# Kernel tuning notes

Hardware: AMD Instinct MI355X
Metric: run time of the kernel (lower is better)

The kernel has to match this reference:

```python
import jax, jax.numpy as jnp
import numpy as np

B, C, H, W = 4, 512, 64, 64
KEY_DIM, VALUE_DIM = 512, 512


def setup_inputs() -> dict:
    key = jax.random.key(0)
    k1, k2, k3, k4 = jax.random.split(key, 4)
    s = 1.0 / np.sqrt(C).astype(np.float32)
    x = jax.random.normal(k1, (B, C, H, W), jnp.float32)
    # torch nn.Linear weights have shape (out_features, in_features)
    Wk = jax.random.normal(k2, (KEY_DIM, C), jnp.float32) * s
    Wq = jax.random.normal(k3, (KEY_DIM, C), jnp.float32) * s
    Wv = jax.random.normal(k4, (VALUE_DIM, C), jnp.float32) * s
    return {"x": x, "Wk": Wk, "Wq": Wq, "Wv": Wv}


def reference(x, Wk, Wq, Wv):
    b, c, h, w = x.shape
    kd = Wk.shape[0]
    n = h * w
    # (b,c,h,w) -> (b, n, c) tokens, matching transpose+flatten in the original
    xt = x.transpose(0, 2, 3, 1).reshape(b, n, c)
    q = xt @ Wq.T  # (b, n, kd)
    k = xt @ Wk.T  # (b, n, kd)
    v = xt @ Wv.T  # (b, n, vd)
    scaling = np.sqrt(float(kd)).astype(np.float32)
    scores = jax.nn.softmax(jnp.einsum('bnd,bmd->bnm', q, k) / scaling, axis=-1)
    # original: output[j] = sum_i values[i] * scores[j, i]  ==  scores @ V
    out = jnp.einsum('bnm,bmv->bnv', scores, v)  # (b, n, vd)
    # original scores_out: sum over dim=0 (query index) of the (n, n) score matrix
    scores_out = scores.sum(axis=1).reshape(b, 1, h, w)
    out = out.reshape(b, h, w, -1).transpose(0, 3, 1, 2)  # (b, vd, h, w)
    return out, scores_out
```

## Files before the change

### kernel.cpp

```cpp
#include <hip/hip_runtime.h>


typedef short bf16x8 __attribute__((ext_vector_type(8)));
typedef float f32x4 __attribute__((ext_vector_type(4)));

#define NTOK 4096
#define DDIM 512
#define NB   4

__device__ __forceinline__ unsigned short f32_bf16(float f) {
  union { float f; unsigned u; } v; v.f = f;
  unsigned r = v.u + 0x7FFFu + ((v.u >> 16) & 1u);
  return (unsigned short)(r >> 16);
}

__device__ __forceinline__ float bf16_f32(short s) {
  union { unsigned u; float f; } v;
  v.u = ((unsigned)(unsigned short)s) << 16;
  return v.f;
}

__global__ __launch_bounds__(256, 4) void qkv_proj(
    const float* __restrict__ x,
    const float* __restrict__ Wq,
    const float* __restrict__ Wk,
    const float* __restrict__ Wv,
    unsigned short* __restrict__ Qt,
    unsigned short* __restrict__ Kf,
    unsigned short* __restrict__ Vt)
{
  const int nt0 = blockIdx.x * 64;
  const int d0  = blockIdx.y * 64;
  const int b   = blockIdx.z;
  const int tid = threadIdx.x;
  const int wave = tid >> 6;
  const int lane = tid & 63;
  const int l15  = lane & 15;
  const int quad = lane >> 4;

  __shared__ __align__(16) unsigned short Xt[64 * 40];
  __shared__ __align__(16) unsigned short Wl[3][64 * 40];

  f32x4 aq[4], ak[4], av[4];
#pragma unroll
  for (int i = 0; i < 4; ++i) {
    aq[i] = (f32x4){0.f,0.f,0.f,0.f};
    ak[i] = (f32x4){0.f,0.f,0.f,0.f};
    av[i] = (f32x4){0.f,0.f,0.f,0.f};
  }

  const float* xb = x + (size_t)b * DDIM * NTOK + nt0;
  const int xn  = tid & 63;
  const int xc8 = tid >> 6;
  const int wc8 = tid & 3;
  const int wdd = tid >> 2;

  for (int cc = 0; cc < DDIM; cc += 32) {
    __syncthreads();
    {
      bf16x8 t;
#pragma unroll
      for (int j = 0; j < 8; ++j)
        t[j] = (short)f32_bf16(xb[(size_t)(cc + xc8 * 8 + j) * NTOK + xn]);
      *(bf16x8*)(&Xt[xn * 40 + xc8 * 8]) = t;
    }
    {
      const float* wsrc[3] = {Wq, Wk, Wv};
#pragma unroll
      for (int m = 0; m < 3; ++m) {
        const float* src = wsrc[m] + (size_t)(d0 + wdd) * DDIM + cc + wc8 * 8;
        bf16x8 t;
#pragma unroll
        for (int j = 0; j < 8; ++j) t[j] = (short)f32_bf16(src[j]);
        *(bf16x8*)(&Wl[m][wdd * 40 + wc8 * 8]) = t;
      }
    }
    __syncthreads();

    bf16x8 xa  = *(const bf16x8*)(&Xt[(wave * 16 + l15) * 40 + quad * 8]);
    bf16x8 wva = *(const bf16x8*)(&Wl[2][(wave * 16 + l15) * 40 + quad * 8]);
#pragma unroll
    for (int nt = 0; nt < 4; ++nt) {
      bf16x8 wqf = *(const bf16x8*)(&Wl[0][(nt * 16 + l15) * 40 + quad * 8]);
      bf16x8 wkf = *(const bf16x8*)(&Wl[1][(nt * 16 + l15) * 40 + quad * 8]);
      bf16x8 xbf = *(const bf16x8*)(&Xt[(nt * 16 + l15) * 40 + quad * 8]);
      aq[nt] = __builtin_amdgcn_mfma_f32_16x16x32_bf16(xa,  wqf, aq[nt], 0, 0, 0);
      ak[nt] = __builtin_amdgcn_mfma_f32_16x16x32_bf16(xa,  wkf, ak[nt], 0, 0, 0);
      av[nt] = __builtin_amdgcn_mfma_f32_16x16x32_bf16(wva, xbf, av[nt], 0, 0, 0);
    }
  }

#pragma unroll
  for (int nt = 0; nt < 4; ++nt) {
#pragma unroll
    for (int r = 0; r < 4; ++r) {
      const int tokq = nt0 + wave * 16 + quad * 4 + r;
      const int dq   = d0 + nt * 16 + l15;
      Qt[((size_t)b * NTOK + tokq) * DDIM + dq] = f32_bf16(aq[nt][r]);
      {
        const int kblk  = (nt0 >> 4) + wave;
        const int dc    = (d0 >> 5) + (nt >> 1);
        const int laneK = ((nt & 1) * 2 + (l15 >> 3)) * 16 + quad * 4 + r;
        Kf[((size_t)(b * 256 + kblk) * 16 + dc) * 512 + laneK * 8 + (l15 & 7)] =
            f32_bf16(ak[nt][r]);
      }
      const int dblk  = (d0 >> 4) + wave;
      const int ic    = (nt0 >> 5) + (nt >> 1);
      const int laneV = ((nt & 1) * 2 + (l15 >> 3)) * 16 + quad * 4 + r;
      Vt[(size_t)b * DDIM * NTOK +
         ((size_t)(dblk * 128 + ic) * 64 + laneV) * 8 + (l15 & 7)] =
          f32_bf16(av[nt][r]);
    }
  }
}

#define SCALE 0.044194173824159216f

__global__ __launch_bounds__(256, 2) void attn_lsum_p(
    const unsigned short* __restrict__ Qt,
    const unsigned short* __restrict__ Kf,
    unsigned short* __restrict__ Pt,
    float* __restrict__ lsum_g)
{
  const int qb = blockIdx.x;
  const int kp = blockIdx.y;
  const int b  = blockIdx.z;
  const int tid  = threadIdx.x;
  const int wave = tid >> 6;
  const int lane = tid & 63;
  const int l15  = lane & 15;
  const int quad = lane >> 4;
  const int q0   = qb * 128 + wave * 32;

  __shared__ __align__(16) unsigned short Klds[64 * 512];

  bf16x8 qf[2][16];
#pragma unroll
  for (int qt = 0; qt < 2; ++qt) {
    const unsigned short* qp =
        Qt + ((size_t)b * NTOK + q0 + qt * 16 + l15) * DDIM + quad * 8;
#pragma unroll
    for (int dc = 0; dc < 16; ++dc) qf[qt][dc] = *(const bf16x8*)(qp + dc * 32);
  }

  unsigned short* Pq = Pt + (size_t)b * NTOK * NTOK +
                       (size_t)(qb * 2 + (wave >> 1)) * 262144;
  const int ntb = (wave & 1) * 2;

  float ls[2][4] = {{0.f,0.f,0.f,0.f},{0.f,0.f,0.f,0.f}};

  for (int kc = 0; kc < 16; ++kc) {
    const int kblk0 = kp * 64 + kc * 4;
    __syncthreads();
    {
      const unsigned short* src = Kf + ((size_t)(b * 256 + kblk0) * 16) * 512;
#pragma unroll
      for (int it = 0; it < 16; ++it) {
        const int idx = (tid + it * 256) * 8;
        *(bf16x8*)(&Klds[idx]) = *(const bf16x8*)(src + idx);
      }
    }
    __syncthreads();

#pragma unroll
    for (int kt = 0; kt < 4; ++kt) {
      const int kabs = kblk0 + kt;
      f32x4 s0 = (f32x4){0.f,0.f,0.f,0.f};
      f32x4 s1 = (f32x4){0.f,0.f,0.f,0.f};
#pragma unroll
      for (int dc = 0; dc < 16; ++dc) {
        const bf16x8 kbf = *(const bf16x8*)(&Klds[(kt * 16 + dc) * 512 + lane * 8]);
        s0 = __builtin_amdgcn_mfma_f32_16x16x32_bf16(qf[0][dc], kbf, s0, 0, 0, 0);
        s1 = __builtin_amdgcn_mfma_f32_16x16x32_bf16(qf[1][dc], kbf, s1, 0, 0, 0);
      }
      const int ic    = kabs >> 1;
      const int lt_hi = ((kabs & 1) * 2 + (l15 >> 3)) * 16;
      const int jj    = l15 & 7;
#pragma unroll
      for (int r = 0; r < 4; ++r) {
        const float e0 = __expf(s0[r] * SCALE);
        const float e1 = __expf(s1[r] * SCALE);
        ls[0][r] += e0;
        ls[1][r] += e1;
        Pq[((size_t)(ic * 4 + ntb) * 64 + lt_hi + quad * 4 + r) * 8 + jj] =
            f32_bf16(e0);
        Pq[((size_t)(ic * 4 + ntb + 1) * 64 + lt_hi + quad * 4 + r) * 8 + jj] =
            f32_bf16(e1);
      }
    }
  }

#pragma unroll
  for (int qt = 0; qt < 2; ++qt)
#pragma unroll
    for (int r = 0; r < 4; ++r) {
      float v = ls[qt][r];
      v += __shfl_xor(v, 1);
      v += __shfl_xor(v, 2);
      v += __shfl_xor(v, 4);
      v += __shfl_xor(v, 8);
      if (l15 == 0)
        unsafeAtomicAdd(&lsum_g[(size_t)b * NTOK + q0 + qt * 16 + quad * 4 + r], v);
    }
}

__global__ __launch_bounds__(256, 4) void attn_pv(
    const unsigned short* __restrict__ Pt,
    const unsigned short* __restrict__ Vt,
    const float* __restrict__ lsum_g,
    float* __restrict__ out,
    float* __restrict__ scores_out)
{
  const int q0b   = blockIdx.x;
  const int dpart = blockIdx.y;
  const int b     = blockIdx.z;
  const int tid  = threadIdx.x;
  const int wave = tid >> 6;
  const int lane = tid & 63;
  const int l15  = lane & 15;
  const int quad = lane >> 4;

  const int dblk0 = dpart * 8 + wave * 2;
  const unsigned short* Pq =
      Pt + (size_t)b * NTOK * NTOK + (size_t)q0b * 262144 + lane * 8;
  const unsigned short* Vp0 =
      Vt + (size_t)b * DDIM * NTOK + (size_t)(dblk0 + 0) * 65536 + lane * 8;
  const unsigned short* Vp1 =
      Vt + (size_t)b * DDIM * NTOK + (size_t)(dblk0 + 1) * 65536 + lane * 8;
  float* scb = scores_out + (size_t)b * NTOK;

  float rlv[4];
#pragma unroll
  for (int nt = 0; nt < 4; ++nt)
    rlv[nt] = 1.0f / lsum_g[(size_t)b * NTOK + q0b * 64 + nt * 16 + l15];

  f32x4 o[2][4];
#pragma unroll
  for (int i = 0; i < 2; ++i)
#pragma unroll
    for (int j = 0; j < 4; ++j) o[i][j] = (f32x4){0.f,0.f,0.f,0.f};

  bf16x8 pA[4], pB[4], vA[2], vB[2];

#define LOADP(D_, IC_)                                                         \
  do {                                                                         \
    _Pragma("unroll") for (int nt = 0; nt < 4; ++nt)                           \
      D_[nt] = *(const bf16x8*)(Pq + (size_t)(IC_)*2048 + nt * 512);           \
  } while (0)

#define LOADV(D_, IC_)                                                         \
  do {                                                                         \
    D_[0] = *(const bf16x8*)(Vp0 + (size_t)(IC_)*512);                         \
    D_[1] = *(const bf16x8*)(Vp1 + (size_t)(IC_)*512);                         \
  } while (0)

#define PV_COMPUTE(P_, V_, IC_)                                                \
  do {                                                                         \
    _Pragma("unroll") for (int mt = 0; mt < 2; ++mt)                           \
      _Pragma("unroll") for (int nt = 0; nt < 4; ++nt)                         \
        o[mt][nt] = __builtin_amdgcn_mfma_f32_16x16x32_bf16(                   \
            V_[mt], P_[nt], o[mt][nt], 0, 0, 0);                               \
    if ((((IC_) >> 5) == dpart) && ((((IC_) >> 3) & 3) == wave)) {             \
      float cj[8];                                                             \
      _Pragma("unroll") for (int j = 0; j < 8; ++j) cj[j] = 0.f;               \
      _Pragma("unroll") for (int nt = 0; nt < 4; ++nt)                         \
        _Pragma("unroll") for (int j = 0; j < 8; ++j)                          \
          cj[j] = fmaf(bf16_f32(P_[nt][j]), rlv[nt], cj[j]);                   \
      _Pragma("unroll") for (int j = 0; j < 8; ++j) {                          \
        float v_ = cj[j];                                                      \
        v_ += __shfl_xor(v_, 1);                                               \
        v_ += __shfl_xor(v_, 2);                                               \
        v_ += __shfl_xor(v_, 4);                                               \
        v_ += __shfl_xor(v_, 8);                                               \
        cj[j] = v_;                                                            \
      }                                                                        \
      if (l15 == 0) {                                                          \
        _Pragma("unroll") for (int j = 0; j < 8; ++j)                          \
          unsafeAtomicAdd(&scb[(IC_)*32 + quad * 8 + j], cj[j]);               \
      }                                                                        \
    }                                                                          \
  } while (0)

  LOADP(pA, 0); LOADV(vA, 0);
  LOADP(pB, 1); LOADV(vB, 1);

  for (int ic = 0; ic < 124; ic += 2) {
    PV_COMPUTE(pA, vA, ic);
    LOADP(pA, ic + 2); LOADV(vA, ic + 2);
    PV_COMPUTE(pB, vB, ic + 1);
    LOADP(pB, ic + 3); LOADV(vB, ic + 3);
  }
  PV_COMPUTE(pA, vA, 124);
  LOADP(pA, 126); LOADV(vA, 126);
  PV_COMPUTE(pB, vB, 125);
  LOADP(pB, 127); LOADV(vB, 127);
  PV_COMPUTE(pA, vA, 126);
  PV_COMPUTE(pB, vB, 127);

#undef LOADP
#undef LOADV
#undef PV_COMPUTE

  float* ob = out + ((size_t)b * DDIM + dpart * 128 + wave * 32) * NTOK + q0b * 64;
#pragma unroll
  for (int mt = 0; mt < 2; ++mt)
#pragma unroll
    for (int nt = 0; nt < 4; ++nt)
#pragma unroll
      for (int r = 0; r < 4; ++r)
        ob[(size_t)(mt * 16 + quad * 4 + r) * NTOK + nt * 16 + l15] =
            o[mt][nt][r] * rlv[nt];
}

extern "C" void kernel_launch(void* const* d_in, const int* in_sizes, int n_in,
                              void* d_out, int out_size, void* d_ws, size_t ws_size,
                              hipStream_t stream) {
  const float* x  = (const float*)d_in[0];
  const float* Wk = (const float*)d_in[1];
  const float* Wq = (const float*)d_in[2];
  const float* Wv = (const float*)d_in[3];

  float* out = (float*)d_out;
  float* scores_out = out + (size_t)NB * DDIM * NTOK;

  const size_t mat_elems = (size_t)NB * NTOK * DDIM;
  unsigned short* Qt = (unsigned short*)d_ws;
  unsigned short* Kf = Qt + mat_elems;
  unsigned short* Vt = Kf + mat_elems;
  float* lbuf = (float*)(Vt + mat_elems);
  unsigned short* Pt = (unsigned short*)(lbuf + (size_t)NB * NTOK);

  hipMemsetAsync(lbuf, 0, (size_t)NB * NTOK * sizeof(float), stream);
  hipMemsetAsync(scores_out, 0, (size_t)NB * NTOK * sizeof(float), stream);

  dim3 g1(NTOK / 64, DDIM / 64, NB);
  qkv_proj<<<g1, 256, 0, stream>>>(x, Wq, Wk, Wv, Qt, Kf, Vt);

  dim3 g2(NTOK / 128, 4, NB);
  attn_lsum_p<<<g2, 256, 0, stream>>>(Qt, Kf, Pt, lbuf);

  dim3 g3(NTOK / 64, 4, NB);
  attn_pv<<<g3, 256, 0, stream>>>(Pt, Vt, lbuf, out, scores_out);
}
```

Before: 404.8 us.

## Widen attn_pv tile to 64 value dims per wave with deeper prefetch

Each wave of the P@V kernel now computes 64 value dimensions instead of 32, and the grid's dpart dimension drops from 4 to 2. Each P tile loaded from global memory is therefore reused across twice as many MFMAs, halving total reads of the large P matrix. The software pipeline also deepens from 2 to 4 stages, and the scores_out ownership mapping is adjusted to match. The cost is many more registers (launch bounds lowered to 2 blocks per SM), so occupancy drops and fewer blocks are launched.

```diff
diff --git a/kernel.cpp b/kernel.cpp
--- a/kernel.cpp
+++ b/kernel.cpp
@@ -204,7 +204,7 @@
     }
 }
 
-__global__ __launch_bounds__(256, 4) void attn_pv(
+__global__ __launch_bounds__(256, 2) void attn_pv(
     const unsigned short* __restrict__ Pt,
     const unsigned short* __restrict__ Vt,
     const float* __restrict__ lsum_g,
@@ -220,27 +220,27 @@
   const int l15  = lane & 15;
   const int quad = lane >> 4;
 
-  const int dblk0 = dpart * 8 + wave * 2;
+  const int dblk0 = dpart * 16 + wave * 4;
   const unsigned short* Pq =
       Pt + (size_t)b * NTOK * NTOK + (size_t)q0b * 262144 + lane * 8;
-  const unsigned short* Vp0 =
-      Vt + (size_t)b * DDIM * NTOK + (size_t)(dblk0 + 0) * 65536 + lane * 8;
-  const unsigned short* Vp1 =
-      Vt + (size_t)b * DDIM * NTOK + (size_t)(dblk0 + 1) * 65536 + lane * 8;
+  const unsigned short* Vb =
+      Vt + (size_t)b * DDIM * NTOK + lane * 8;
   float* scb = scores_out + (size_t)b * NTOK;
+  const int sown = dpart * 4 + wave;
 
   float rlv[4];
 #pragma unroll
   for (int nt = 0; nt < 4; ++nt)
     rlv[nt] = 1.0f / lsum_g[(size_t)b * NTOK + q0b * 64 + nt * 16 + l15];
 
-  f32x4 o[2][4];
-#pragma unroll
-  for (int i = 0; i < 2; ++i)
+  f32x4 o[4][4];
+#pragma unroll
+  for (int i = 0; i < 4; ++i)
 #pragma unroll
     for (int j = 0; j < 4; ++j) o[i][j] = (f32x4){0.f,0.f,0.f,0.f};
 
-  bf16x8 pA[4], pB[4], vA[2], vB[2];
+  bf16x8 p0[4], p1[4], p2[4], p3[4];
+  bf16x8 v0[4], v1[4], v2[4], v3[4];
 
 #define LOADP(D_, IC_)                                                         \
   do {                                                                         \
@@ -250,17 +250,18 @@
 
 #define LOADV(D_, IC_)                                                         \
   do {                                                                         \
-    D_[0] = *(const bf16x8*)(Vp0 + (size_t)(IC_)*512);                         \
-    D_[1] = *(const bf16x8*)(Vp1 + (size_t)(IC_)*512);                         \
+    _Pragma("unroll") for (int mt = 0; mt < 4; ++mt)                           \
+      D_[mt] = *(const bf16x8*)(Vb + (size_t)(dblk0 + mt) * 65536 +            \
+                                (size_t)(IC_)*512);                            \
   } while (0)
 
-#define PV_COMPUTE(P_, V_, IC_)                                                \
+#define COMP(P_, V_, IC_)                                                      \
   do {                                                                         \
-    _Pragma("unroll") for (int mt = 0; mt < 2; ++mt)                           \
+    _Pragma("unroll") for (int mt = 0; mt < 4; ++mt)                           \
       _Pragma("unroll") for (int nt = 0; nt < 4; ++nt)                         \
         o[mt][nt] = __builtin_amdgcn_mfma_f32_16x16x32_bf16(                   \
             V_[mt], P_[nt], o[mt][nt], 0, 0, 0);                               \
-    if ((((IC_) >> 5) == dpart) && ((((IC_) >> 3) & 3) == wave)) {             \
+    if (((IC_) >> 4) == sown) {                                                \
       float cj[8];                                                             \
       _Pragma("unroll") for (int j = 0; j < 8; ++j) cj[j] = 0.f;               \
       _Pragma("unroll") for (int nt = 0; nt < 4; ++nt)                         \
@@ -281,29 +282,29 @@
     }                                                                          \
   } while (0)
 
-  LOADP(pA, 0); LOADV(vA, 0);
-  LOADP(pB, 1); LOADV(vB, 1);
-
-  for (int ic = 0; ic < 124; ic += 2) {
-    PV_COMPUTE(pA, vA, ic);
-    LOADP(pA, ic + 2); LOADV(vA, ic + 2);
-    PV_COMPUTE(pB, vB, ic + 1);
-    LOADP(pB, ic + 3); LOADV(vB, ic + 3);
-  }
-  PV_COMPUTE(pA, vA, 124);
-  LOADP(pA, 126); LOADV(vA, 126);
-  PV_COMPUTE(pB, vB, 125);
-  LOADP(pB, 127); LOADV(vB, 127);
-  PV_COMPUTE(pA, vA, 126);
-  PV_COMPUTE(pB, vB, 127);
+  LOADP(p0, 0); LOADV(v0, 0);
+  LOADP(p1, 1); LOADV(v1, 1);
+  LOADP(p2, 2); LOADV(v2, 2);
+  LOADP(p3, 3); LOADV(v3, 3);
+
+  for (int ic = 0; ic < 124; ic += 4) {
+    COMP(p0, v0, ic);     LOADP(p0, ic + 4); LOADV(v0, ic + 4);
+    COMP(p1, v1, ic + 1); LOADP(p1, ic + 5); LOADV(v1, ic + 5);
+    COMP(p2, v2, ic + 2); LOADP(p2, ic + 6); LOADV(v2, ic + 6);
+    COMP(p3, v3, ic + 3); LOADP(p3, ic + 7); LOADV(v3, ic + 7);
+  }
+  COMP(p0, v0, 124);
+  COMP(p1, v1, 125);
+  COMP(p2, v2, 126);
+  COMP(p3, v3, 127);
 
 #undef LOADP
 #undef LOADV
-#undef PV_COMPUTE
-
-  float* ob = out + ((size_t)b * DDIM + dpart * 128 + wave * 32) * NTOK + q0b * 64;
-#pragma unroll
-  for (int mt = 0; mt < 2; ++mt)
+#undef COMP
+
+  float* ob = out + ((size_t)b * DDIM + dpart * 256 + wave * 64) * NTOK + q0b * 64;
+#pragma unroll
+  for (int mt = 0; mt < 4; ++mt)
 #pragma unroll
     for (int nt = 0; nt < 4; ++nt)
 #pragma unroll
@@ -339,6 +340,6 @@
   dim3 g2(NTOK / 128, 4, NB);
   attn_lsum_p<<<g2, 256, 0, stream>>>(Qt, Kf, Pt, lbuf);
 
-  dim3 g3(NTOK / 64, 4, NB);
+  dim3 g3(NTOK / 64, 2, NB);
   attn_pv<<<g3, 256, 0, stream>>>(Pt, Vt, lbuf, out, scores_out);
 }
```

Result: faster. 385.7 us (-4.7%).
